# Performance work log

Measured on AMD Instinct MI355X. Metric: run time of the kernel, lower is better.

Reference implementation:

```python
import jax, jax.numpy as jnp
import numpy as np

B, S, H, D = 4, 2048, 16, 64
E = H * D  # embed_dim = 1024


def setup_inputs() -> dict:
    key = jax.random.key(0)
    kq, kk, kv, kw, kb = jax.random.split(key, 5)
    query = jax.random.normal(kq, (B, S, H, D), dtype=jnp.float32)
    key_t = jax.random.normal(kk, (B, S, H, D), dtype=jnp.float32)
    value = jax.random.normal(kv, (B, S, H, D), dtype=jnp.float32)
    qkv_proj = jnp.zeros((1,), dtype=jnp.float32)  # unused arg in original forward
    # causal mask (0 = masked), matching masked_fill(attn_mask == 0, -inf)
    attn_mask = jnp.tril(jnp.ones((S, S), dtype=jnp.int32))
    bound = 1.0 / np.sqrt(E)
    out_w = jax.random.uniform(kw, (E, E), jnp.float32, -bound, bound)
    out_b = jax.random.uniform(kb, (E,), jnp.float32, -bound, bound)
    return {"query": query, "key": key_t, "value": value, "qkv_proj": qkv_proj,
            "attn_mask": attn_mask, "out_w": out_w, "out_b": out_b}


def reference(query, key, value, qkv_proj, attn_mask, out_w, out_b):
    # flatten heads: module does single-head attention over embed_dim
    q = query.reshape(B, S, E) * (float(E) ** -0.5)  # scaling uses embed_dim, per source
    k = key.reshape(B, S, E)
    v = value.reshape(B, S, E)
    scores = jnp.einsum('bqe,bke->bqk', q, k)  # [B,S,S]
    scores = jnp.where(attn_mask[None, :, :] == 0, -jnp.inf, scores)
    # safe softmax: subtract max, exp, normalize
    probs = jax.nn.softmax(scores, axis=-1)
    attn_out = jnp.einsum('bqk,bke->bqe', probs, v)  # [B,S,E]
    return attn_out @ out_w.T + out_b
```

## Files before the change

### kernel.cpp

```cpp
#include <hip/hip_runtime.h>


typedef __attribute__((ext_vector_type(8))) short bf16x8;
typedef __attribute__((ext_vector_type(4))) float floatx4;

#define MFMA16(a, b, c) __builtin_amdgcn_mfma_f32_16x16x32_bf16((a), (b), (c), 0, 0, 0)

#define B_ 4
#define S_ 2048
#define E_ 1024

static __device__ __forceinline__ unsigned short f2bf(float f) {
  unsigned int u = __float_as_uint(f);
  u += 0x7FFFu + ((u >> 16) & 1u);
  return (unsigned short)(u >> 16);
}

#define STAGE_TILE_64(dst, srcbase, LD, k0, w, l)                              \
  _Pragma("unroll")                                                            \
  for (int i_ = 0; i_ < 4; ++i_) {                                             \
    int c_ = i_ * 256 + (w) * 64 + (l);                                        \
    int row_ = c_ >> 3, cg_ = c_ & 7;                                          \
    int col_ = (cg_ ^ (row_ & 7)) * 8;                                         \
    __builtin_amdgcn_global_load_lds(                                          \
        (const __attribute__((address_space(1))) unsigned int*)((srcbase) +    \
            (size_t)row_ * (LD) + (k0) + col_),                                \
        (__attribute__((address_space(3))) unsigned int*)((dst) +              \
            (size_t)(i_ * 256 + (w) * 64) * 8),                                \
        16, 0, 0);                                                             \
  }

static __device__ __forceinline__ const bf16x8* frag_at(
    const unsigned short* base, int row, int cg) {
  return (const bf16x8*)(base + (size_t)row * 64 + ((cg ^ (row & 7)) * 8));
}

static __device__ __forceinline__ void cvt8(const float* __restrict__ src,
                                            unsigned short* __restrict__ dst,
                                            float sc) {
  float4 x0 = *(const float4*)src;
  float4 x1 = *(const float4*)(src + 4);
  bf16x8 o;
  o[0] = f2bf(x0.x * sc); o[1] = f2bf(x0.y * sc);
  o[2] = f2bf(x0.z * sc); o[3] = f2bf(x0.w * sc);
  o[4] = f2bf(x1.x * sc); o[5] = f2bf(x1.y * sc);
  o[6] = f2bf(x1.z * sc); o[7] = f2bf(x1.w * sc);
  *(bf16x8*)dst = o;
}

__global__ __launch_bounds__(256) void cvt_qk_kernel(
    const float* __restrict__ Q, const float* __restrict__ K,
    unsigned short* __restrict__ Qbf, unsigned short* __restrict__ Kbf) {
  const int bid = blockIdx.x;
  const int qside = bid < 4096;
  const size_t i8 = ((size_t)(qside ? bid : bid - 4096) * 256 + threadIdx.x) * 8;
  if (qside) cvt8(Q + i8, Qbf + i8, 0.03125f);
  else       cvt8(K + i8, Kbf + i8, 1.0f);
}

__global__ __launch_bounds__(256, 4) void qk_cvtvw_kernel(
    const unsigned short* __restrict__ A,
    const unsigned short* __restrict__ Bw,
    unsigned short* __restrict__ SP,
    float* __restrict__ rsp,
    const float* __restrict__ V, const float* __restrict__ W,
    unsigned short* __restrict__ Vbf, unsigned short* __restrict__ Wbf) {
  __shared__ unsigned short At[128 * 64];
  __shared__ unsigned short Bt[128 * 64];
  __shared__ float rs_l[2][128];
  const int bid0 = blockIdx.x;

  if (bid0 >= 544) {
    const int t = (bid0 - 544) * 256 + threadIdx.x;
#pragma unroll
    for (int k = 0; k < 8; ++k) {
      int u = t + k * 147456;
      if (u < 1048576) {
        cvt8(V + (size_t)u * 8, Vbf + (size_t)u * 8, 1.0f);
      } else {
        size_t uw = (size_t)(u - 1048576) * 8;
        cvt8(W + uw, Wbf + uw, 1.0f);
      }
    }
    return;
  }

  const int bid = (bid0 & 7) * 68 + (bid0 >> 3);
  const int b = bid / 136;
  const int ti = bid - b * 136;
  float fr = sqrtf(8.0f * (float)ti + 1.0f);
  int trow = (int)((fr - 1.0f) * 0.5f);
  if ((trow + 1) * (trow + 2) / 2 <= ti) ++trow;
  else if (trow * (trow + 1) / 2 > ti) --trow;
  const int tcol = ti - trow * (trow + 1) / 2;
  const int bm = trow * 128, bn = tcol * 128;

  const int tid = threadIdx.x;
  const int w = tid >> 6, l = tid & 63;
  const int l15 = l & 15, l4 = l >> 4;
  const int wr = w >> 1, wc = w & 1;
  const unsigned short* Ab = A + (size_t)b * S_ * E_ + (size_t)bm * E_;
  const unsigned short* Bb = Bw + (size_t)b * S_ * E_ + (size_t)bn * E_;

  floatx4 acc[4][4];
#pragma unroll
  for (int m = 0; m < 4; ++m)
#pragma unroll
    for (int n = 0; n < 4; ++n) acc[m][n] = (floatx4)0.0f;

  for (int k0 = 0; k0 < E_; k0 += 64) {
    STAGE_TILE_64(At, Ab, E_, k0, w, l)
    STAGE_TILE_64(Bt, Bb, E_, k0, w, l)
    __syncthreads();
#pragma unroll
    for (int h = 0; h < 2; ++h) {
      bf16x8 af[4], bfv[4];
#pragma unroll
      for (int mf = 0; mf < 4; ++mf)
        af[mf] = *frag_at(At, wr * 64 + mf * 16 + l15, h * 4 + l4);
#pragma unroll
      for (int nf = 0; nf < 4; ++nf)
        bfv[nf] = *frag_at(Bt, wc * 64 + nf * 16 + l15, h * 4 + l4);
#pragma unroll
      for (int mf = 0; mf < 4; ++mf)
#pragma unroll
        for (int nf = 0; nf < 4; ++nf)
          acc[mf][nf] = MFMA16(af[mf], bfv[nf], acc[mf][nf]);
    }
    __syncthreads();
  }

  float ps[16];
#pragma unroll
  for (int i = 0; i < 16; ++i) ps[i] = 0.0f;
  unsigned short* Cb = SP + (size_t)b * S_ * S_;
#pragma unroll
  for (int mf = 0; mf < 4; ++mf)
#pragma unroll
    for (int nf = 0; nf < 4; ++nf)
#pragma unroll
      for (int r = 0; r < 4; ++r) {
        int row = bm + wr * 64 + mf * 16 + l4 * 4 + r;
        int col = bn + wc * 64 + nf * 16 + l15;
        float p = (col <= row) ? __expf(acc[mf][nf][r]) : 0.0f;
        ps[mf * 4 + r] += p;
        Cb[(size_t)row * S_ + col] = f2bf(p);
      }
#pragma unroll
  for (int i = 0; i < 16; ++i) {
    float s = ps[i];
    s += __shfl_xor(s, 1);
    s += __shfl_xor(s, 2);
    s += __shfl_xor(s, 4);
    s += __shfl_xor(s, 8);
    ps[i] = s;
  }
  if (l15 == 0) {
#pragma unroll
    for (int mf = 0; mf < 4; ++mf)
#pragma unroll
      for (int r = 0; r < 4; ++r)
        rs_l[wc][wr * 64 + mf * 16 + l4 * 4 + r] = ps[mf * 4 + r];
  }
  __syncthreads();
  if (tid < 128)
    rsp[((size_t)(b * S_ + bm + tid)) * 17 + tcol] = rs_l[0][tid] + rs_l[1][tid];
}

__global__ __launch_bounds__(256, 3) void vw_kernel(
    const unsigned short* __restrict__ Wbf,
    const unsigned short* __restrict__ Vbf,
    unsigned short* __restrict__ Ut) {
  __shared__ unsigned short At[128 * 64];
  __shared__ unsigned short Bt[128 * 64];
  const int bid0 = blockIdx.x;
  const int bid = (bid0 & 7) * 64 + (bid0 >> 3);
  const int b = bid >> 7;
  const int mt = (bid >> 4) & 7;
  const int nt = bid & 15;
  const int bm = mt * 128, bn = nt * 128;

  const int tid = threadIdx.x;
  const int w = tid >> 6, l = tid & 63;
  const int l15 = l & 15, l4 = l >> 4;
  const int wr = w >> 1, wc = w & 1;
  const unsigned short* Ab = Wbf + (size_t)bm * E_;
  const unsigned short* Bb = Vbf + (size_t)b * S_ * E_ + (size_t)bn * E_;

  floatx4 acc[4][4];
#pragma unroll
  for (int m = 0; m < 4; ++m)
#pragma unroll
    for (int n = 0; n < 4; ++n) acc[m][n] = (floatx4)0.0f;

  for (int k0 = 0; k0 < E_; k0 += 64) {
    STAGE_TILE_64(At, Ab, E_, k0, w, l)
    STAGE_TILE_64(Bt, Bb, E_, k0, w, l)
    __syncthreads();
#pragma unroll
    for (int h = 0; h < 2; ++h) {
      bf16x8 af[4], bfv[4];
#pragma unroll
      for (int mf = 0; mf < 4; ++mf)
        af[mf] = *frag_at(At, wr * 64 + mf * 16 + l15, h * 4 + l4);
#pragma unroll
      for (int nf = 0; nf < 4; ++nf)
        bfv[nf] = *frag_at(Bt, wc * 64 + nf * 16 + l15, h * 4 + l4);
#pragma unroll
      for (int mf = 0; mf < 4; ++mf)
#pragma unroll
        for (int nf = 0; nf < 4; ++nf)
          acc[mf][nf] = MFMA16(af[mf], bfv[nf], acc[mf][nf]);
    }
    __syncthreads();
  }

  unsigned short* Cb = Ut + (size_t)b * E_ * S_;
#pragma unroll
  for (int mf = 0; mf < 4; ++mf)
#pragma unroll
    for (int nf = 0; nf < 4; ++nf)
#pragma unroll
      for (int r = 0; r < 4; ++r) {
        int row = bm + wr * 64 + mf * 16 + l4 * 4 + r;
        int col = bn + wc * 64 + nf * 16 + l15;
        Cb[(size_t)row * S_ + col] = f2bf(acc[mf][nf][r]);
      }
}

__global__ __launch_bounds__(256, 3) void pu_kernel(
    const unsigned short* __restrict__ P,
    const unsigned short* __restrict__ Ut,
    const float* __restrict__ rsp,
    const float* __restrict__ bias,
    float* __restrict__ out) {
  __shared__ unsigned short At[128 * 64];
  __shared__ unsigned short Bt[128 * 64];
  __shared__ float inv_l[128];
  const int bid0 = blockIdx.x;
  const int x = bid0 & 7;
  const int j = bid0 >> 3;
  const int b = x >> 1;
  const int nt = (x & 1) * 4 + (j & 3);
  const int r2 = j >> 2;
  const int mt = (r2 < 8) ? r2 : 23 - r2;
  const int bm = mt * 128, bn = nt * 128;

  const int tid = threadIdx.x;
  const int w = tid >> 6, l = tid & 63;
  const int l15 = l & 15, l4 = l >> 4;
  const int wr = w >> 1, wc = w & 1;

  {
    float* srd = (float*)At;
    const float4* rp4 =
        (const float4*)(rsp + ((size_t)(b * S_ + bm)) * 17);
    for (int i = tid; i < 544; i += 256) ((float4*)srd)[i] = rp4[i];
    __syncthreads();
    if (tid < 128) {
      float s = 0.0f;
      for (int t = 0; t <= mt; ++t) s += srd[tid * 17 + t];
      inv_l[tid] = 1.0f / s;
    }
    __syncthreads();
  }

  const unsigned short* Ab = P + (size_t)b * S_ * S_ + (size_t)bm * S_;
  const unsigned short* Bb = Ut + (size_t)b * E_ * S_ + (size_t)bn * S_;

  floatx4 acc[4][4];
#pragma unroll
  for (int m = 0; m < 4; ++m)
#pragma unroll
    for (int n = 0; n < 4; ++n) acc[m][n] = (floatx4)0.0f;

  const int kmax = (mt + 1) * 128;
  for (int k0 = 0; k0 < kmax; k0 += 64) {
    STAGE_TILE_64(At, Ab, S_, k0, w, l)
    STAGE_TILE_64(Bt, Bb, S_, k0, w, l)
    __syncthreads();
#pragma unroll
    for (int h = 0; h < 2; ++h) {
      bf16x8 af[4], bfv[4];
#pragma unroll
      for (int mf = 0; mf < 4; ++mf)
        af[mf] = *frag_at(At, wr * 64 + mf * 16 + l15, h * 4 + l4);
#pragma unroll
      for (int nf = 0; nf < 4; ++nf)
        bfv[nf] = *frag_at(Bt, wc * 64 + nf * 16 + l15, h * 4 + l4);
#pragma unroll
      for (int mf = 0; mf < 4; ++mf)
#pragma unroll
        for (int nf = 0; nf < 4; ++nf)
          acc[mf][nf] = MFMA16(af[mf], bfv[nf], acc[mf][nf]);
    }
    __syncthreads();
  }

  float* Cb = out + (size_t)b * S_ * E_;
  float bv[4];
#pragma unroll
  for (int nf = 0; nf < 4; ++nf) bv[nf] = bias[bn + wc * 64 + nf * 16 + l15];
#pragma unroll
  for (int mf = 0; mf < 4; ++mf) {
    float inv[4];
#pragma unroll
    for (int r = 0; r < 4; ++r)
      inv[r] = inv_l[wr * 64 + mf * 16 + l4 * 4 + r];
#pragma unroll
    for (int nf = 0; nf < 4; ++nf)
#pragma unroll
      for (int r = 0; r < 4; ++r) {
        int row = bm + wr * 64 + mf * 16 + l4 * 4 + r;
        int col = bn + wc * 64 + nf * 16 + l15;
        Cb[(size_t)row * E_ + col] = acc[mf][nf][r] * inv[r] + bv[nf];
      }
  }
}

extern "C" void kernel_launch(void* const* d_in, const int* in_sizes, int n_in,
                              void* d_out, int out_size, void* d_ws, size_t ws_size,
                              hipStream_t stream) {
  const float* Q    = (const float*)d_in[0];
  const float* Kf   = (const float*)d_in[1];
  const float* V    = (const float*)d_in[2];
  const float* W    = (const float*)d_in[5];
  const float* bias = (const float*)d_in[6];
  float* out = (float*)d_out;
  (void)ws_size;

  char* ws = (char*)d_ws;
  unsigned short* Qbf = (unsigned short*)(ws);
  unsigned short* Kbf = (unsigned short*)(ws + (size_t)(16u << 20));
  unsigned short* Vbf = (unsigned short*)(ws + (size_t)(32u << 20));
  unsigned short* Wbf = (unsigned short*)(ws + (size_t)(48u << 20));
  unsigned short* SP  = (unsigned short*)(ws + (size_t)(50u << 20));
  float*          rsp = (float*)(ws + (size_t)(82u << 20));
  unsigned short* Ut = Qbf;

  cvt_qk_kernel<<<8192, 256, 0, stream>>>(Q, Kf, Qbf, Kbf);
  qk_cvtvw_kernel<<<544 + 576, 256, 0, stream>>>(Qbf, Kbf, SP, rsp,
                                                 V, W, Vbf, Wbf);
  vw_kernel<<<512, 256, 0, stream>>>(Wbf, Vbf, Ut);
  pu_kernel<<<512, 256, 0, stream>>>(SP, Ut, rsp, bias, out);
}
```

Baseline: 104.9 us.

## Convert all inputs upfront and co-schedule QK and VW GEMMs in one launch

Moves the V and W bf16 conversion into the first conversion kernel, so the second launch no longer carries extra conversion blocks. It then merges the QK^T score GEMM and the W·V^T GEMM into a single launch when the workspace is large enough, writing Ut to a separate buffer instead of aliasing Qbf. This removes one kernel launch and lets the two independent GEMMs share the GPU. The cost is extra workspace, plus a fallback path of two launches when the workspace is small.

```diff
diff --git a/kernel.cpp b/kernel.cpp
--- a/kernel.cpp
+++ b/kernel.cpp
@@ -48,40 +48,88 @@
   *(bf16x8*)dst = o;
 }
 
-__global__ __launch_bounds__(256) void cvt_qk_kernel(
+__global__ __launch_bounds__(256) void cvt_all_kernel(
     const float* __restrict__ Q, const float* __restrict__ K,
-    unsigned short* __restrict__ Qbf, unsigned short* __restrict__ Kbf) {
+    const float* __restrict__ V, const float* __restrict__ W,
+    unsigned short* __restrict__ Qbf, unsigned short* __restrict__ Kbf,
+    unsigned short* __restrict__ Vbf, unsigned short* __restrict__ Wbf) {
   const int bid = blockIdx.x;
-  const int qside = bid < 4096;
-  const size_t i8 = ((size_t)(qside ? bid : bid - 4096) * 256 + threadIdx.x) * 8;
-  if (qside) cvt8(Q + i8, Qbf + i8, 0.03125f);
-  else       cvt8(K + i8, Kbf + i8, 1.0f);
-}
-
-__global__ __launch_bounds__(256, 4) void qk_cvtvw_kernel(
+  const float* src; unsigned short* dst; float sc = 1.0f; int base;
+  if (bid < 4096)       { src = Q; dst = Qbf; sc = 0.03125f; base = bid; }
+  else if (bid < 8192)  { src = K; dst = Kbf; base = bid - 4096; }
+  else if (bid < 12288) { src = V; dst = Vbf; base = bid - 8192; }
+  else                  { src = W; dst = Wbf; base = bid - 12288; }
+  const size_t i8 = ((size_t)base * 256 + threadIdx.x) * 8;
+  cvt8(src + i8, dst + i8, sc);
+}
+
+__global__ __launch_bounds__(256, 4) void qk_vw_kernel(
     const unsigned short* __restrict__ A,
     const unsigned short* __restrict__ Bw,
     unsigned short* __restrict__ SP,
     float* __restrict__ rsp,
-    const float* __restrict__ V, const float* __restrict__ W,
-    unsigned short* __restrict__ Vbf, unsigned short* __restrict__ Wbf) {
+    const unsigned short* __restrict__ Wbf,
+    const unsigned short* __restrict__ Vbf,
+    unsigned short* __restrict__ Ut,
+    int vw_base) {
   __shared__ unsigned short At[128 * 64];
   __shared__ unsigned short Bt[128 * 64];
   __shared__ float rs_l[2][128];
   const int bid0 = blockIdx.x;
-
-  if (bid0 >= 544) {
-    const int t = (bid0 - 544) * 256 + threadIdx.x;
-#pragma unroll
-    for (int k = 0; k < 8; ++k) {
-      int u = t + k * 147456;
-      if (u < 1048576) {
-        cvt8(V + (size_t)u * 8, Vbf + (size_t)u * 8, 1.0f);
-      } else {
-        size_t uw = (size_t)(u - 1048576) * 8;
-        cvt8(W + uw, Wbf + uw, 1.0f);
+  const int tid = threadIdx.x;
+  const int w = tid >> 6, l = tid & 63;
+  const int l15 = l & 15, l4 = l >> 4;
+  const int wr = w >> 1, wc = w & 1;
+
+  if (bid0 >= vw_base) {
+    const int vbid = bid0 - vw_base;
+    const int bid = (vbid & 7) * 64 + (vbid >> 3);
+    const int b = bid >> 7;
+    const int mt = (bid >> 4) & 7;
+    const int nt = bid & 15;
+    const int bm = mt * 128, bn = nt * 128;
+    const unsigned short* Ab = Wbf + (size_t)bm * E_;
+    const unsigned short* Bb = Vbf + (size_t)b * S_ * E_ + (size_t)bn * E_;
+
+    floatx4 acc[4][4];
+#pragma unroll
+    for (int m = 0; m < 4; ++m)
+#pragma unroll
+      for (int n = 0; n < 4; ++n) acc[m][n] = (floatx4)0.0f;
+
+    for (int k0 = 0; k0 < E_; k0 += 64) {
+      STAGE_TILE_64(At, Ab, E_, k0, w, l)
+      STAGE_TILE_64(Bt, Bb, E_, k0, w, l)
+      __syncthreads();
+#pragma unroll
+      for (int h = 0; h < 2; ++h) {
+        bf16x8 af[4], bfv[4];
+#pragma unroll
+        for (int mf = 0; mf < 4; ++mf)
+          af[mf] = *frag_at(At, wr * 64 + mf * 16 + l15, h * 4 + l4);
+#pragma unroll
+        for (int nf = 0; nf < 4; ++nf)
+          bfv[nf] = *frag_at(Bt, wc * 64 + nf * 16 + l15, h * 4 + l4);
+#pragma unroll
+        for (int mf = 0; mf < 4; ++mf)
+#pragma unroll
+          for (int nf = 0; nf < 4; ++nf)
+            acc[mf][nf] = MFMA16(af[mf], bfv[nf], acc[mf][nf]);
       }
+      __syncthreads();
     }
+
+    unsigned short* Cb = Ut + (size_t)b * E_ * S_;
+#pragma unroll
+    for (int mf = 0; mf < 4; ++mf)
+#pragma unroll
+      for (int nf = 0; nf < 4; ++nf)
+#pragma unroll
+        for (int r = 0; r < 4; ++r) {
+          int row = bm + wr * 64 + mf * 16 + l4 * 4 + r;
+          int col = bn + wc * 64 + nf * 16 + l15;
+          Cb[(size_t)row * S_ + col] = f2bf(acc[mf][nf][r]);
+        }
     return;
   }
 
@@ -95,10 +143,6 @@
   const int tcol = ti - trow * (trow + 1) / 2;
   const int bm = trow * 128, bn = tcol * 128;
 
-  const int tid = threadIdx.x;
-  const int w = tid >> 6, l = tid & 63;
-  const int l15 = l & 15, l4 = l >> 4;
-  const int wr = w >> 1, wc = w & 1;
   const unsigned short* Ab = A + (size_t)b * S_ * E_ + (size_t)bm * E_;
   const unsigned short* Bb = Bw + (size_t)b * S_ * E_ + (size_t)bn * E_;
 
@@ -165,67 +209,6 @@
   __syncthreads();
   if (tid < 128)
     rsp[((size_t)(b * S_ + bm + tid)) * 17 + tcol] = rs_l[0][tid] + rs_l[1][tid];
-}
-
-__global__ __launch_bounds__(256, 3) void vw_kernel(
-    const unsigned short* __restrict__ Wbf,
-    const unsigned short* __restrict__ Vbf,
-    unsigned short* __restrict__ Ut) {
-  __shared__ unsigned short At[128 * 64];
-  __shared__ unsigned short Bt[128 * 64];
-  const int bid0 = blockIdx.x;
-  const int bid = (bid0 & 7) * 64 + (bid0 >> 3);
-  const int b = bid >> 7;
-  const int mt = (bid >> 4) & 7;
-  const int nt = bid & 15;
-  const int bm = mt * 128, bn = nt * 128;
-
-  const int tid = threadIdx.x;
-  const int w = tid >> 6, l = tid & 63;
-  const int l15 = l & 15, l4 = l >> 4;
-  const int wr = w >> 1, wc = w & 1;
-  const unsigned short* Ab = Wbf + (size_t)bm * E_;
-  const unsigned short* Bb = Vbf + (size_t)b * S_ * E_ + (size_t)bn * E_;
-
-  floatx4 acc[4][4];
-#pragma unroll
-  for (int m = 0; m < 4; ++m)
-#pragma unroll
-    for (int n = 0; n < 4; ++n) acc[m][n] = (floatx4)0.0f;
-
-  for (int k0 = 0; k0 < E_; k0 += 64) {
-    STAGE_TILE_64(At, Ab, E_, k0, w, l)
-    STAGE_TILE_64(Bt, Bb, E_, k0, w, l)
-    __syncthreads();
-#pragma unroll
-    for (int h = 0; h < 2; ++h) {
-      bf16x8 af[4], bfv[4];
-#pragma unroll
-      for (int mf = 0; mf < 4; ++mf)
-        af[mf] = *frag_at(At, wr * 64 + mf * 16 + l15, h * 4 + l4);
-#pragma unroll
-      for (int nf = 0; nf < 4; ++nf)
-        bfv[nf] = *frag_at(Bt, wc * 64 + nf * 16 + l15, h * 4 + l4);
-#pragma unroll
-      for (int mf = 0; mf < 4; ++mf)
-#pragma unroll
-        for (int nf = 0; nf < 4; ++nf)
-          acc[mf][nf] = MFMA16(af[mf], bfv[nf], acc[mf][nf]);
-    }
-    __syncthreads();
-  }
-
-  unsigned short* Cb = Ut + (size_t)b * E_ * S_;
-#pragma unroll
-  for (int mf = 0; mf < 4; ++mf)
-#pragma unroll
-    for (int nf = 0; nf < 4; ++nf)
-#pragma unroll
-      for (int r = 0; r < 4; ++r) {
-        int row = bm + wr * 64 + mf * 16 + l4 * 4 + r;
-        int col = bn + wc * 64 + nf * 16 + l15;
-        Cb[(size_t)row * S_ + col] = f2bf(acc[mf][nf][r]);
-      }
 }
 
 __global__ __launch_bounds__(256, 3) void pu_kernel(
@@ -327,7 +310,6 @@
   const float* W    = (const float*)d_in[5];
   const float* bias = (const float*)d_in[6];
   float* out = (float*)d_out;
-  (void)ws_size;
 
   char* ws = (char*)d_ws;
   unsigned short* Qbf = (unsigned short*)(ws);
@@ -336,11 +318,16 @@
   unsigned short* Wbf = (unsigned short*)(ws + (size_t)(48u << 20));
   unsigned short* SP  = (unsigned short*)(ws + (size_t)(50u << 20));
   float*          rsp = (float*)(ws + (size_t)(82u << 20));
-  unsigned short* Ut = Qbf;
-
-  cvt_qk_kernel<<<8192, 256, 0, stream>>>(Q, Kf, Qbf, Kbf);
-  qk_cvtvw_kernel<<<544 + 576, 256, 0, stream>>>(Qbf, Kbf, SP, rsp,
-                                                 V, W, Vbf, Wbf);
-  vw_kernel<<<512, 256, 0, stream>>>(Wbf, Vbf, Ut);
+  const bool bigws = ws_size >= ((size_t)101u << 20);
+  unsigned short* Ut = bigws ? (unsigned short*)(ws + (size_t)(84u << 20))
+                             : Qbf;
+
+  cvt_all_kernel<<<12800, 256, 0, stream>>>(Q, Kf, V, W, Qbf, Kbf, Vbf, Wbf);
+  if (bigws) {
+    qk_vw_kernel<<<1056, 256, 0, stream>>>(Qbf, Kbf, SP, rsp, Wbf, Vbf, Ut, 544);
+  } else {
+    qk_vw_kernel<<<544, 256, 0, stream>>>(Qbf, Kbf, SP, rsp, Wbf, Vbf, Ut, 9999);
+    qk_vw_kernel<<<512, 256, 0, stream>>>(Qbf, Kbf, SP, rsp, Wbf, Vbf, Ut, 0);
+  }
   pu_kernel<<<512, 256, 0, stream>>>(SP, Ut, rsp, bias, out);
 }
```

After: 106.2 us. Within noise of the previous version (+1.2%).
